# Kernel tuning notes

Hardware: AMD Instinct MI355X
Metric: run time of the kernel (lower is better)

## Reference

```python
import jax, jax.numpy as jnp
import numpy as np

D_MODEL = 512
D_FF = 512
N_EXPERTS = 16
TOP_K = 3
BATCH, SEQ = 1, 2048


def setup_inputs() -> dict:
    key = jax.random.key(0)
    ks = jax.random.split(key, 6)
    x = jax.random.normal(ks[0], (BATCH, SEQ, D_MODEL), dtype=jnp.float32)
    # router gate (std=0.01 per _init_weights)
    gate_w = 0.01 * jax.random.normal(ks[1], (N_EXPERTS, D_MODEL), dtype=jnp.float32)
    expert_bias = jnp.zeros((N_EXPERTS,), dtype=jnp.float32)  # registered buffer, zeros
    # shared SwiGLU expert (std=0.02)
    shared_gate_up = 0.02 * jax.random.normal(ks[2], (2 * D_FF, D_MODEL), dtype=jnp.float32)
    shared_down = 0.02 * jax.random.normal(ks[3], (D_MODEL, D_FF), dtype=jnp.float32)
    # batched routed experts (std=0.02)
    expert_gate_up = 0.02 * jax.random.normal(ks[4], (N_EXPERTS, 2 * D_FF, D_MODEL), dtype=jnp.float32)
    expert_down = 0.02 * jax.random.normal(ks[5], (N_EXPERTS, D_MODEL, D_FF), dtype=jnp.float32)
    return {
        "x": x,
        "gate_w": gate_w,
        "expert_bias": expert_bias,
        "shared_gate_up": shared_gate_up,
        "shared_down": shared_down,
        "expert_gate_up": expert_gate_up,
        "expert_down": expert_down,
    }


def _swiglu(combined):
    gate, up = jnp.split(combined, 2, axis=-1)
    return jax.nn.silu(gate) * up


def reference(x, gate_w, expert_bias, shared_gate_up, shared_down, expert_gate_up, expert_down):
    B, S, D = x.shape
    xf = x.reshape(-1, D)  # [T, D]

    # ---- shared expert (always active) ----
    shared_out = _swiglu(xf @ shared_gate_up.T) @ shared_down.T  # [T, D]

    # ---- router: sigmoid affinity + bias-adjusted top-k ----
    logits = xf @ gate_w.T  # [T, E]
    affinity = jax.nn.sigmoid(logits)
    routing_scores = affinity + expert_bias  # expert_bias buffer (zeros)
    _, sel = jax.lax.top_k(routing_scores, TOP_K)  # [T, K]
    sel_aff = jnp.take_along_axis(affinity, sel, axis=1)  # [T, K]
    gating = sel_aff / (sel_aff.sum(axis=-1, keepdims=True) + 1e-9)  # [T, K]

    # ---- routed experts: per-token SwiGLU with the token's expert weights ----
    # Computed densely per expert then gathered; identical math to the
    # per-token weight-gather in BatchedExperts.
    combined = jnp.einsum('td,efd->tef', xf, expert_gate_up)  # [T, E, 2F]
    hidden = _swiglu(combined)  # [T, E, F]
    expert_out = jnp.einsum('tef,edf->ted', hidden, expert_down)  # [T, E, D]
    sel_out = jnp.take_along_axis(expert_out, sel[:, :, None], axis=1)  # [T, K, D]
    routed_out = jnp.einsum('tk,tkd->td', gating, sel_out)  # [T, D]

    out = shared_out + routed_out  # dropout p=0.0 -> identity
    return out.reshape(B, S, D)
```

## Files before the change

kernel.cpp:

```cpp
#include <hip/hip_runtime.h>

#define T_TOK 2048
#define DM    512
#define DFF   512
#define NE    16

typedef __attribute__((ext_vector_type(8))) short bf16x8;
typedef __attribute__((ext_vector_type(4))) float f32x4;
typedef __attribute__((ext_vector_type(8))) unsigned short us8;

__device__ __forceinline__ unsigned short f2bf(float f) {
  unsigned int u = __float_as_uint(f);
  u += 0x7fffu + ((u >> 16) & 1u);
  return (unsigned short)(u >> 16);
}

__device__ __forceinline__ void dma16(const unsigned short* g, unsigned short* l) {
  __builtin_amdgcn_global_load_lds(
      (const __attribute__((address_space(1))) unsigned int*)g,
      (__attribute__((address_space(3))) unsigned int*)l, 16, 0, 0);
}

#define LDSOFF(row, chunk) ((((row) << 7) + ((((chunk) ^ ((row) & 7))) << 4)))

#define MFMA(a,b,c) __builtin_amdgcn_mfma_f32_16x16x32_bf16((a),(b),(c),0,0,0)

__global__ __launch_bounds__(256) void prep_kernel(
    const float* __restrict__ x, const float* __restrict__ gw,
    const float* __restrict__ bias, int* __restrict__ counts,
    int* __restrict__ list, float* __restrict__ wgt,
    const float* __restrict__ sgu, const float* __restrict__ sdn,
    const float* __restrict__ egu, const float* __restrict__ edn,
    unsigned short* __restrict__ xb,   unsigned short* __restrict__ sgub,
    unsigned short* __restrict__ sdnb, unsigned short* __restrict__ egub,
    unsigned short* __restrict__ ednb, float* __restrict__ out)
{
  const int tid = threadIdx.x;
  if (blockIdx.x >= 512) {
    const int cb = blockIdx.x - 512;
    const int ct = cb * 256 + tid;
    const int CT = 7040 * 256;
    const float4 z4 = {0.f, 0.f, 0.f, 0.f};
    for (int i = ct; i < 262144; i += CT) ((float4*)out)[i] = z4;
    int g = ct;
    const float* s; unsigned short* d; int l;
    if      (g <  131072) { s = x;   d = xb;   l = g;           }
    else if (g <  196608) { s = sgu; d = sgub; l = g -  131072; }
    else if (g <  229376) { s = sdn; d = sdnb; l = g -  196608; }
    else if (g < 1277952) { s = egu; d = egub; l = g -  229376; }
    else                  { s = edn; d = ednb; l = g - 1277952; }
    const float* p = s + (size_t)l * 8;
    float4 v0 = *(const float4*)p;
    float4 v1 = *(const float4*)(p + 4);
    us8 o;
    o[0]=f2bf(v0.x); o[1]=f2bf(v0.y); o[2]=f2bf(v0.z); o[3]=f2bf(v0.w);
    o[4]=f2bf(v1.x); o[5]=f2bf(v1.y); o[6]=f2bf(v1.z); o[7]=f2bf(v1.w);
    *(us8*)(d + (size_t)l * 8) = o;
    return;
  }

  __shared__ float lg[4][16];
  __shared__ int bcnt[16], bbase[16];
  __shared__ int sel_s[4][3], pos_s[4][3];
  __shared__ float g_s[4][3];

  const int w = tid >> 6, lane = tid & 63;
  if (tid < 16) bcnt[tid] = 0;
  const int tok = blockIdx.x * 4 + w;
  const int e = lane & 15, part = lane >> 4;

  const float* xr = x + (size_t)tok * DM + part * 128;
  const float* wr = gw + (size_t)e * DM + part * 128;
  float acc = 0.f;
  #pragma unroll 8
  for (int i = 0; i < 128; i += 4) {
    float4 xv = *(const float4*)(xr + i);
    float4 wv = *(const float4*)(wr + i);
    acc += xv.x*wv.x + xv.y*wv.y + xv.z*wv.z + xv.w*wv.w;
  }
  acc += __shfl_xor(acc, 16);
  acc += __shfl_xor(acc, 32);
  if (lane < 16) lg[w][lane] = 1.f / (1.f + __expf(-acc));
  __syncthreads();

  if (tid < 4) {
    float aff[16], sc[16];
    #pragma unroll
    for (int i = 0; i < 16; ++i) { aff[i] = lg[tid][i]; sc[i] = aff[i] + bias[i]; }
    int sel[3]; float sa[3]; float sum = 0.f;
    #pragma unroll
    for (int k = 0; k < 3; ++k) {
      float best = -1e30f; int bi = 0;
      for (int i = 0; i < 16; ++i) {
        bool used = false;
        for (int j = 0; j < k; ++j) used |= (sel[j] == i);
        if (!used && sc[i] > best) { best = sc[i]; bi = i; }
      }
      sel[k] = bi; sa[k] = aff[bi]; sum += aff[bi];
    }
    float inv = 1.f / (sum + 1e-9f);
    #pragma unroll
    for (int k = 0; k < 3; ++k) {
      int p = atomicAdd(&bcnt[sel[k]], 1);
      sel_s[tid][k] = sel[k]; pos_s[tid][k] = p; g_s[tid][k] = sa[k] * inv;
    }
  }
  __syncthreads();
  if (tid < 16) bbase[tid] = atomicAdd(&counts[tid], bcnt[tid]);
  __syncthreads();
  if (tid < 4) {
    #pragma unroll
    for (int k = 0; k < 3; ++k) {
      int E = sel_s[tid][k];
      int p = bbase[E] + pos_s[tid][k];
      list[E * T_TOK + p] = blockIdx.x * 4 + tid;
      wgt [E * T_TOK + p] = g_s[tid][k];
    }
  }
}

__global__ __launch_bounds__(256, 2) void gemm1_fused(
    const unsigned short* __restrict__ X, const unsigned short* __restrict__ Wsh,
    const unsigned short* __restrict__ Wex, unsigned short* __restrict__ Hall,
    const int* __restrict__ counts, const int* __restrict__ list)
{
  __shared__ unsigned short SA[2][128][64];
  __shared__ unsigned short SG[2][64][64];
  __shared__ unsigned short SU[2][64][64];

  const int n0 = blockIdx.x * 64;
  const int mt = blockIdx.y, z = blockIdx.z;
  int cnt, hb; const unsigned short* W;
  if (z == 0) { cnt = T_TOK; hb = 0; W = Wsh; }
  else {
    const int e = z - 1;
    cnt = counts[e];
    if (mt * 128 >= cnt) return;
    hb = T_TOK;
    for (int i = 0; i < e; ++i) hb += counts[i];
    W = Wex + (size_t)e * (2 * DFF * DM);
  }

  const int tid = threadIdx.x, w = tid >> 6, lane = tid & 63;
  const int rsub = lane >> 3;
  const int cch  = (lane & 7) ^ rsub;
  const unsigned short* ga[4];
  #pragma unroll
  for (int q = 0; q < 4; ++q) {
    int ra = mt * 128 + q * 32 + w * 8 + rsub;
    int rc = ra < cnt ? ra : cnt - 1;
    int tokr = (z == 0) ? rc : list[(z - 1) * T_TOK + rc];
    ga[q] = X + (size_t)tokr * DM + cch * 8;
  }
  const unsigned short *gg[2], *gu[2];
  #pragma unroll
  for (int q = 0; q < 2; ++q) {
    int rb = n0 + q * 32 + w * 8 + rsub;
    gg[q] = W + (size_t)rb * DM + cch * 8;
    gu[q] = W + (size_t)(DFF + rb) * DM + cch * 8;
  }
  unsigned short* lA[2][4]; unsigned short* lG[2][2]; unsigned short* lU[2][2];
  #pragma unroll
  for (int b = 0; b < 2; ++b) {
    #pragma unroll
    for (int q = 0; q < 4; ++q) lA[b][q] = &SA[b][q * 32 + w * 8][0];
    #pragma unroll
    for (int q = 0; q < 2; ++q) {
      lG[b][q] = &SG[b][q * 32 + w * 8][0];
      lU[b][q] = &SU[b][q * 32 + w * 8][0];
    }
  }

  const int wm = (w & 1) * 64;
  const int wn = (w >> 1) * 32;
  const int lr = lane & 15, qd = lane >> 4;
  const char* const sa = (const char*)SA;
  const char* const sg = (const char*)SG;
  const char* const su = (const char*)SU;

  const f32x4 z4 = {0.f, 0.f, 0.f, 0.f};
  f32x4 accg[4][2], accu[4][2];
  #pragma unroll
  for (int i = 0; i < 4; ++i)
    #pragma unroll
    for (int j = 0; j < 2; ++j) { accg[i][j] = z4; accu[i][j] = z4; }

  #pragma unroll
  for (int q = 0; q < 4; ++q) dma16(ga[q], lA[0][q]);
  #pragma unroll
  for (int q = 0; q < 2; ++q) { dma16(gg[q], lG[0][q]); dma16(gu[q], lU[0][q]); }

  #pragma unroll
  for (int i = 0; i < DM / 64; ++i) {
    const int b = i & 1;
    __syncthreads();
    if (i + 1 < DM / 64) {
      const int k1 = (i + 1) * 64, nb = b ^ 1;
      #pragma unroll
      for (int q = 0; q < 4; ++q) dma16(ga[q] + k1, lA[nb][q]);
      #pragma unroll
      for (int q = 0; q < 2; ++q) {
        dma16(gg[q] + k1, lG[nb][q]);
        dma16(gu[q] + k1, lU[nb][q]);
      }
    }
    const int boA = b * 16384;
    const int boB = b * 8192;
    #pragma unroll
    for (int ks = 0; ks < 2; ++ks) {
      const int ch = ks * 4 + qd;
      bf16x8 a[4], g[2], u[2];
      #pragma unroll
      for (int sm = 0; sm < 4; ++sm)
        a[sm] = *(const bf16x8*)(sa + boA + LDSOFF(wm + sm * 16 + lr, ch));
      #pragma unroll
      for (int sn = 0; sn < 2; ++sn) {
        g[sn] = *(const bf16x8*)(sg + boB + LDSOFF(wn + sn * 16 + lr, ch));
        u[sn] = *(const bf16x8*)(su + boB + LDSOFF(wn + sn * 16 + lr, ch));
      }
      #pragma unroll
      for (int sm = 0; sm < 4; ++sm)
        #pragma unroll
        for (int sn = 0; sn < 2; ++sn) {
          accg[sm][sn] = MFMA(a[sm], g[sn], accg[sm][sn]);
          accu[sm][sn] = MFMA(a[sm], u[sn], accu[sm][sn]);
        }
    }
  }

  #pragma unroll
  for (int sm = 0; sm < 4; ++sm)
    #pragma unroll
    for (int sn = 0; sn < 2; ++sn) {
      const int col = n0 + wn + sn * 16 + lr;
      #pragma unroll
      for (int r = 0; r < 4; ++r) {
        const int ent = mt * 128 + wm + sm * 16 + qd * 4 + r;
        if (ent < cnt) {
          float g = accg[sm][sn][r];
          float u = accu[sm][sn][r];
          float h = (g / (1.f + __expf(-g))) * u;
          Hall[(size_t)(hb + ent) * DFF + col] = f2bf(h);
        }
      }
    }
}

__global__ __launch_bounds__(256, 3) void gemm2_fused(
    const unsigned short* __restrict__ Hall, const unsigned short* __restrict__ Wsh,
    const unsigned short* __restrict__ Wex, float* __restrict__ out,
    const int* __restrict__ counts, const int* __restrict__ list,
    const float* __restrict__ wgt)
{
  __shared__ unsigned short SA[2][128][64];
  __shared__ unsigned short SB[2][64][64];

  const int n0 = blockIdx.x * 64;
  const int mt = blockIdx.y, z = blockIdx.z;
  int cnt, hb; const unsigned short* W;
  if (z == 0) { cnt = T_TOK; hb = 0; W = Wsh; }
  else {
    const int e = z - 1;
    cnt = counts[e];
    if (mt * 128 >= cnt) return;
    hb = T_TOK;
    for (int i = 0; i < e; ++i) hb += counts[i];
    W = Wex + (size_t)e * (DM * DFF);
  }

  const int tid = threadIdx.x, w = tid >> 6, lane = tid & 63;
  const int rsub = lane >> 3;
  const int cch  = (lane & 7) ^ rsub;
  const unsigned short* ga[4];
  #pragma unroll
  for (int q = 0; q < 4; ++q) {
    int ra = mt * 128 + q * 32 + w * 8 + rsub;
    int rc = ra < cnt ? ra : cnt - 1;
    ga[q] = Hall + (size_t)(hb + rc) * DFF + cch * 8;
  }
  const unsigned short* gb[2];
  #pragma unroll
  for (int q = 0; q < 2; ++q)
    gb[q] = W + (size_t)(n0 + q * 32 + w * 8 + rsub) * DFF + cch * 8;
  unsigned short* lA[2][4]; unsigned short* lB[2][2];
  #pragma unroll
  for (int b = 0; b < 2; ++b) {
    #pragma unroll
    for (int q = 0; q < 4; ++q) lA[b][q] = &SA[b][q * 32 + w * 8][0];
    #pragma unroll
    for (int q = 0; q < 2; ++q) lB[b][q] = &SB[b][q * 32 + w * 8][0];
  }

  const int wm = (w & 1) * 64;
  const int wn = (w >> 1) * 32;
  const int lr = lane & 15, qd = lane >> 4;
  const char* const sa = (const char*)SA;
  const char* const sb = (const char*)SB;

  const f32x4 z4 = {0.f, 0.f, 0.f, 0.f};
  f32x4 acc[4][2];
  #pragma unroll
  for (int i = 0; i < 4; ++i)
    #pragma unroll
    for (int j = 0; j < 2; ++j) acc[i][j] = z4;

  #pragma unroll
  for (int q = 0; q < 4; ++q) dma16(ga[q], lA[0][q]);
  #pragma unroll
  for (int q = 0; q < 2; ++q) dma16(gb[q], lB[0][q]);

  #pragma unroll
  for (int i = 0; i < DFF / 64; ++i) {
    const int b = i & 1;
    __syncthreads();
    if (i + 1 < DFF / 64) {
      const int k1 = (i + 1) * 64, nb = b ^ 1;
      #pragma unroll
      for (int q = 0; q < 4; ++q) dma16(ga[q] + k1, lA[nb][q]);
      #pragma unroll
      for (int q = 0; q < 2; ++q) dma16(gb[q] + k1, lB[nb][q]);
    }
    const int boA = b * 16384;
    const int boB = b * 8192;
    #pragma unroll
    for (int ks = 0; ks < 2; ++ks) {
      const int ch = ks * 4 + qd;
      bf16x8 a[4], bb[2];
      #pragma unroll
      for (int sm = 0; sm < 4; ++sm)
        a[sm] = *(const bf16x8*)(sa + boA + LDSOFF(wm + sm * 16 + lr, ch));
      #pragma unroll
      for (int sn = 0; sn < 2; ++sn)
        bb[sn] = *(const bf16x8*)(sb + boB + LDSOFF(wn + sn * 16 + lr, ch));
      #pragma unroll
      for (int sm = 0; sm < 4; ++sm)
        #pragma unroll
        for (int sn = 0; sn < 2; ++sn)
          acc[sm][sn] = MFMA(a[sm], bb[sn], acc[sm][sn]);
    }
  }

  #pragma unroll
  for (int sm = 0; sm < 4; ++sm)
    #pragma unroll
    for (int sn = 0; sn < 2; ++sn) {
      const int col = n0 + wn + sn * 16 + lr;
      #pragma unroll
      for (int r = 0; r < 4; ++r) {
        const int ent = mt * 128 + wm + sm * 16 + qd * 4 + r;
        if (ent < cnt) {
          float v = acc[sm][sn][r];
          if (z == 0) {
            atomicAdd(out + (size_t)ent * DM + col, v);
          } else {
            const int   tok = list[(z - 1) * T_TOK + ent];
            const float g   = wgt [(z - 1) * T_TOK + ent];
            atomicAdd(out + (size_t)tok * DM + col, g * v);
          }
        }
      }
    }
}

extern "C" void kernel_launch(void* const* d_in, const int* in_sizes, int n_in,
                              void* d_out, int out_size, void* d_ws, size_t ws_size,
                              hipStream_t stream) {
  const float* x    = (const float*)d_in[0];
  const float* gw   = (const float*)d_in[1];
  const float* bias = (const float*)d_in[2];
  const float* sgu  = (const float*)d_in[3];
  const float* sdn  = (const float*)d_in[4];
  const float* egu  = (const float*)d_in[5];
  const float* edn  = (const float*)d_in[6];
  float* out = (float*)d_out;

  char* ws = (char*)d_ws;
  int*            counts = (int*)(ws + 0);
  int*            list   = (int*)(ws + 64);
  float*          wgt    = (float*)(ws + 131136);
  unsigned short* Hall   = (unsigned short*)(ws + 262208);
  unsigned short* xb     = (unsigned short*)(ws + 8650816);
  unsigned short* sgub   = (unsigned short*)(ws + 10747968);
  unsigned short* sdnb   = (unsigned short*)(ws + 11796544);
  unsigned short* egub   = (unsigned short*)(ws + 12320832);
  unsigned short* ednb   = (unsigned short*)(ws + 29098048);
  const size_t need = 37486656;
  if (ws_size < need) return;

  hipMemsetAsync(counts, 0, 64, stream);
  prep_kernel<<<512 + 7040, 256, 0, stream>>>(
      x, gw, bias, counts, list, wgt, sgu, sdn, egu, edn,
      xb, sgub, sdnb, egub, ednb, out);
  gemm1_fused<<<dim3(8, 16, NE + 1), 256, 0, stream>>>(xb, sgub, egub, Hall, counts, list);
  gemm2_fused<<<dim3(8, 16, NE + 1), 256, 0, stream>>>(Hall, sdnb, ednb, out, counts, list, wgt);
}
```

Measured before the change: 168.4 us.

## Fuse fp32-to-bf16 conversion into GEMM tile loads, drop pre-conversion pass

Removes the separate pass in the prep kernel that converted x and all expert/shared weights to bf16 in workspace. The GEMM kernels now load fp32 tiles into registers, pack them to bf16 and store them into swizzled LDS themselves, replacing the async global-to-LDS DMA for those operands. This saves a full read and write of about 36MB of converted data. In exchange the GEMMs read twice the bytes per tile, repeat the conversion for every tile that reuses a weight or activation row, and lose the asynchronous LDS DMA path, with more register pressure.

```diff
diff --git a/kernel.cpp b/kernel.cpp
--- a/kernel.cpp
+++ b/kernel.cpp
@@ -15,6 +15,13 @@
   return (unsigned short)(u >> 16);
 }
 
+__device__ __forceinline__ us8 pack8(float4 v0, float4 v1) {
+  us8 o;
+  o[0]=f2bf(v0.x); o[1]=f2bf(v0.y); o[2]=f2bf(v0.z); o[3]=f2bf(v0.w);
+  o[4]=f2bf(v1.x); o[5]=f2bf(v1.y); o[6]=f2bf(v1.z); o[7]=f2bf(v1.w);
+  return o;
+}
+
 __device__ __forceinline__ void dma16(const unsigned short* g, unsigned short* l) {
   __builtin_amdgcn_global_load_lds(
       (const __attribute__((address_space(1))) unsigned int*)g,
@@ -29,34 +36,14 @@
     const float* __restrict__ x, const float* __restrict__ gw,
     const float* __restrict__ bias, int* __restrict__ counts,
     int* __restrict__ list, float* __restrict__ wgt,
-    const float* __restrict__ sgu, const float* __restrict__ sdn,
-    const float* __restrict__ egu, const float* __restrict__ edn,
-    unsigned short* __restrict__ xb,   unsigned short* __restrict__ sgub,
-    unsigned short* __restrict__ sdnb, unsigned short* __restrict__ egub,
-    unsigned short* __restrict__ ednb, float* __restrict__ out)
+    float* __restrict__ out)
 {
   const int tid = threadIdx.x;
-  if (blockIdx.x >= 512) {
-    const int cb = blockIdx.x - 512;
-    const int ct = cb * 256 + tid;
-    const int CT = 7040 * 256;
+  {
+    const int g = blockIdx.x * 256 + tid;
     const float4 z4 = {0.f, 0.f, 0.f, 0.f};
-    for (int i = ct; i < 262144; i += CT) ((float4*)out)[i] = z4;
-    int g = ct;
-    const float* s; unsigned short* d; int l;
-    if      (g <  131072) { s = x;   d = xb;   l = g;           }
-    else if (g <  196608) { s = sgu; d = sgub; l = g -  131072; }
-    else if (g <  229376) { s = sdn; d = sdnb; l = g -  196608; }
-    else if (g < 1277952) { s = egu; d = egub; l = g -  229376; }
-    else                  { s = edn; d = ednb; l = g - 1277952; }
-    const float* p = s + (size_t)l * 8;
-    float4 v0 = *(const float4*)p;
-    float4 v1 = *(const float4*)(p + 4);
-    us8 o;
-    o[0]=f2bf(v0.x); o[1]=f2bf(v0.y); o[2]=f2bf(v0.z); o[3]=f2bf(v0.w);
-    o[4]=f2bf(v1.x); o[5]=f2bf(v1.y); o[6]=f2bf(v1.z); o[7]=f2bf(v1.w);
-    *(us8*)(d + (size_t)l * 8) = o;
-    return;
+    ((float4*)out)[g] = z4;
+    ((float4*)out)[g + 131072] = z4;
   }
 
   __shared__ float lg[4][16];
@@ -120,8 +107,8 @@
 }
 
 __global__ __launch_bounds__(256, 2) void gemm1_fused(
-    const unsigned short* __restrict__ X, const unsigned short* __restrict__ Wsh,
-    const unsigned short* __restrict__ Wex, unsigned short* __restrict__ Hall,
+    const float* __restrict__ X, const float* __restrict__ Wsh,
+    const float* __restrict__ Wex, unsigned short* __restrict__ Hall,
     const int* __restrict__ counts, const int* __restrict__ list)
 {
   __shared__ unsigned short SA[2][128][64];
@@ -130,7 +117,7 @@
 
   const int n0 = blockIdx.x * 64;
   const int mt = blockIdx.y, z = blockIdx.z;
-  int cnt, hb; const unsigned short* W;
+  int cnt, hb; const float* W;
   if (z == 0) { cnt = T_TOK; hb = 0; W = Wsh; }
   else {
     const int e = z - 1;
@@ -143,31 +130,33 @@
 
   const int tid = threadIdx.x, w = tid >> 6, lane = tid & 63;
   const int rsub = lane >> 3;
-  const int cch  = (lane & 7) ^ rsub;
-  const unsigned short* ga[4];
+  const int c    = lane & 7;
+
+  const float* gA[4];
+  unsigned short* lA[2][4];
   #pragma unroll
   for (int q = 0; q < 4; ++q) {
-    int ra = mt * 128 + q * 32 + w * 8 + rsub;
+    const int rA = q * 32 + w * 8 + rsub;
+    int ra = mt * 128 + rA;
     int rc = ra < cnt ? ra : cnt - 1;
     int tokr = (z == 0) ? rc : list[(z - 1) * T_TOK + rc];
-    ga[q] = X + (size_t)tokr * DM + cch * 8;
-  }
-  const unsigned short *gg[2], *gu[2];
+    gA[q] = X + (size_t)tokr * DM + c * 8;
+    #pragma unroll
+    for (int b = 0; b < 2; ++b)
+      lA[b][q] = &SA[b][rA][0] + ((c ^ (rA & 7)) << 3);
+  }
+  const float *gG[2], *gU[2];
+  unsigned short *lG[2][2], *lU[2][2];
   #pragma unroll
   for (int q = 0; q < 2; ++q) {
-    int rb = n0 + q * 32 + w * 8 + rsub;
-    gg[q] = W + (size_t)rb * DM + cch * 8;
-    gu[q] = W + (size_t)(DFF + rb) * DM + cch * 8;
-  }
-  unsigned short* lA[2][4]; unsigned short* lG[2][2]; unsigned short* lU[2][2];
-  #pragma unroll
-  for (int b = 0; b < 2; ++b) {
-    #pragma unroll
-    for (int q = 0; q < 4; ++q) lA[b][q] = &SA[b][q * 32 + w * 8][0];
-    #pragma unroll
-    for (int q = 0; q < 2; ++q) {
-      lG[b][q] = &SG[b][q * 32 + w * 8][0];
-      lU[b][q] = &SU[b][q * 32 + w * 8][0];
+    const int rB = q * 32 + w * 8 + rsub;
+    const int rb = n0 + rB;
+    gG[q] = W + (size_t)rb * DM + c * 8;
+    gU[q] = W + (size_t)(DFF + rb) * DM + c * 8;
+    #pragma unroll
+    for (int b = 0; b < 2; ++b) {
+      lG[b][q] = &SG[b][rB][0] + ((c ^ (rB & 7)) << 3);
+      lU[b][q] = &SU[b][rB][0] + ((c ^ (rB & 7)) << 3);
     }
   }
 
@@ -185,23 +174,42 @@
     #pragma unroll
     for (int j = 0; j < 2; ++j) { accg[i][j] = z4; accu[i][j] = z4; }
 
-  #pragma unroll
-  for (int q = 0; q < 4; ++q) dma16(ga[q], lA[0][q]);
-  #pragma unroll
-  for (int q = 0; q < 2; ++q) { dma16(gg[q], lG[0][q]); dma16(gu[q], lU[0][q]); }
+  float4 av0[4], av1[4], gv0[2], gv1[2], uv0[2], uv1[2];
+
+  #pragma unroll
+  for (int q = 0; q < 4; ++q) {
+    av0[q] = *(const float4*)gA[q]; av1[q] = *(const float4*)(gA[q] + 4);
+  }
+  #pragma unroll
+  for (int q = 0; q < 2; ++q) {
+    gv0[q] = *(const float4*)gG[q]; gv1[q] = *(const float4*)(gG[q] + 4);
+    uv0[q] = *(const float4*)gU[q]; uv1[q] = *(const float4*)(gU[q] + 4);
+  }
+  #pragma unroll
+  for (int q = 0; q < 4; ++q) *(us8*)lA[0][q] = pack8(av0[q], av1[q]);
+  #pragma unroll
+  for (int q = 0; q < 2; ++q) {
+    *(us8*)lG[0][q] = pack8(gv0[q], gv1[q]);
+    *(us8*)lU[0][q] = pack8(uv0[q], uv1[q]);
+  }
 
   #pragma unroll
   for (int i = 0; i < DM / 64; ++i) {
     const int b = i & 1;
     __syncthreads();
     if (i + 1 < DM / 64) {
-      const int k1 = (i + 1) * 64, nb = b ^ 1;
-      #pragma unroll
-      for (int q = 0; q < 4; ++q) dma16(ga[q] + k1, lA[nb][q]);
+      const int k1 = (i + 1) * 64;
+      #pragma unroll
+      for (int q = 0; q < 4; ++q) {
+        av0[q] = *(const float4*)(gA[q] + k1);
+        av1[q] = *(const float4*)(gA[q] + k1 + 4);
+      }
       #pragma unroll
       for (int q = 0; q < 2; ++q) {
-        dma16(gg[q] + k1, lG[nb][q]);
-        dma16(gu[q] + k1, lU[nb][q]);
+        gv0[q] = *(const float4*)(gG[q] + k1);
+        gv1[q] = *(const float4*)(gG[q] + k1 + 4);
+        uv0[q] = *(const float4*)(gU[q] + k1);
+        uv1[q] = *(const float4*)(gU[q] + k1 + 4);
       }
     }
     const int boA = b * 16384;
@@ -225,6 +233,16 @@
           accg[sm][sn] = MFMA(a[sm], g[sn], accg[sm][sn]);
           accu[sm][sn] = MFMA(a[sm], u[sn], accu[sm][sn]);
         }
+    }
+    if (i + 1 < DM / 64) {
+      const int nb = b ^ 1;
+      #pragma unroll
+      for (int q = 0; q < 4; ++q) *(us8*)lA[nb][q] = pack8(av0[q], av1[q]);
+      #pragma unroll
+      for (int q = 0; q < 2; ++q) {
+        *(us8*)lG[nb][q] = pack8(gv0[q], gv1[q]);
+        *(us8*)lU[nb][q] = pack8(uv0[q], uv1[q]);
+      }
     }
   }
 
@@ -247,8 +265,8 @@
 }
 
 __global__ __launch_bounds__(256, 3) void gemm2_fused(
-    const unsigned short* __restrict__ Hall, const unsigned short* __restrict__ Wsh,
-    const unsigned short* __restrict__ Wex, float* __restrict__ out,
+    const unsigned short* __restrict__ Hall, const float* __restrict__ Wsh,
+    const float* __restrict__ Wex, float* __restrict__ out,
     const int* __restrict__ counts, const int* __restrict__ list,
     const float* __restrict__ wgt)
 {
@@ -257,7 +275,7 @@
 
   const int n0 = blockIdx.x * 64;
   const int mt = blockIdx.y, z = blockIdx.z;
-  int cnt, hb; const unsigned short* W;
+  int cnt, hb; const float* W;
   if (z == 0) { cnt = T_TOK; hb = 0; W = Wsh; }
   else {
     const int e = z - 1;
@@ -270,25 +288,29 @@
 
   const int tid = threadIdx.x, w = tid >> 6, lane = tid & 63;
   const int rsub = lane >> 3;
-  const int cch  = (lane & 7) ^ rsub;
+  const int c    = lane & 7;
+  const int cch  = c ^ rsub;
+
   const unsigned short* ga[4];
+  unsigned short* lA[2][4];
   #pragma unroll
   for (int q = 0; q < 4; ++q) {
     int ra = mt * 128 + q * 32 + w * 8 + rsub;
     int rc = ra < cnt ? ra : cnt - 1;
     ga[q] = Hall + (size_t)(hb + rc) * DFF + cch * 8;
-  }
-  const unsigned short* gb[2];
-  #pragma unroll
-  for (int q = 0; q < 2; ++q)
-    gb[q] = W + (size_t)(n0 + q * 32 + w * 8 + rsub) * DFF + cch * 8;
-  unsigned short* lA[2][4]; unsigned short* lB[2][2];
-  #pragma unroll
-  for (int b = 0; b < 2; ++b) {
-    #pragma unroll
-    for (int q = 0; q < 4; ++q) lA[b][q] = &SA[b][q * 32 + w * 8][0];
-    #pragma unroll
-    for (int q = 0; q < 2; ++q) lB[b][q] = &SB[b][q * 32 + w * 8][0];
+    #pragma unroll
+    for (int b = 0; b < 2; ++b)
+      lA[b][q] = &SA[b][q * 32 + w * 8][0];
+  }
+  const float* gB[2];
+  unsigned short* lB[2][2];
+  #pragma unroll
+  for (int q = 0; q < 2; ++q) {
+    const int rB = q * 32 + w * 8 + rsub;
+    gB[q] = W + (size_t)(n0 + rB) * DFF + c * 8;
+    #pragma unroll
+    for (int b = 0; b < 2; ++b)
+      lB[b][q] = &SB[b][rB][0] + ((c ^ (rB & 7)) << 3);
   }
 
   const int wm = (w & 1) * 64;
@@ -304,10 +326,16 @@
     #pragma unroll
     for (int j = 0; j < 2; ++j) acc[i][j] = z4;
 
+  float4 bv0[2], bv1[2];
+
   #pragma unroll
   for (int q = 0; q < 4; ++q) dma16(ga[q], lA[0][q]);
   #pragma unroll
-  for (int q = 0; q < 2; ++q) dma16(gb[q], lB[0][q]);
+  for (int q = 0; q < 2; ++q) {
+    bv0[q] = *(const float4*)gB[q]; bv1[q] = *(const float4*)(gB[q] + 4);
+  }
+  #pragma unroll
+  for (int q = 0; q < 2; ++q) *(us8*)lB[0][q] = pack8(bv0[q], bv1[q]);
 
   #pragma unroll
   for (int i = 0; i < DFF / 64; ++i) {
@@ -318,7 +346,10 @@
       #pragma unroll
       for (int q = 0; q < 4; ++q) dma16(ga[q] + k1, lA[nb][q]);
       #pragma unroll
-      for (int q = 0; q < 2; ++q) dma16(gb[q] + k1, lB[nb][q]);
+      for (int q = 0; q < 2; ++q) {
+        bv0[q] = *(const float4*)(gB[q] + k1);
+        bv1[q] = *(const float4*)(gB[q] + k1 + 4);
+      }
     }
     const int boA = b * 16384;
     const int boB = b * 8192;
@@ -337,6 +368,11 @@
         #pragma unroll
         for (int sn = 0; sn < 2; ++sn)
           acc[sm][sn] = MFMA(a[sm], bb[sn], acc[sm][sn]);
+    }
+    if (i + 1 < DFF / 64) {
+      const int nb = b ^ 1;
+      #pragma unroll
+      for (int q = 0; q < 2; ++q) *(us8*)lB[nb][q] = pack8(bv0[q], bv1[q]);
     }
   }
 
@@ -379,18 +415,11 @@
   int*            list   = (int*)(ws + 64);
   float*          wgt    = (float*)(ws + 131136);
   unsigned short* Hall   = (unsigned short*)(ws + 262208);
-  unsigned short* xb     = (unsigned short*)(ws + 8650816);
-  unsigned short* sgub   = (unsigned short*)(ws + 10747968);
-  unsigned short* sdnb   = (unsigned short*)(ws + 11796544);
-  unsigned short* egub   = (unsigned short*)(ws + 12320832);
-  unsigned short* ednb   = (unsigned short*)(ws + 29098048);
-  const size_t need = 37486656;
+  const size_t need = 8650816;
   if (ws_size < need) return;
 
   hipMemsetAsync(counts, 0, 64, stream);
-  prep_kernel<<<512 + 7040, 256, 0, stream>>>(
-      x, gw, bias, counts, list, wgt, sgu, sdn, egu, edn,
-      xb, sgub, sdnb, egub, ednb, out);
-  gemm1_fused<<<dim3(8, 16, NE + 1), 256, 0, stream>>>(xb, sgub, egub, Hall, counts, list);
-  gemm2_fused<<<dim3(8, 16, NE + 1), 256, 0, stream>>>(Hall, sdnb, ednb, out, counts, list, wgt);
-}
+  prep_kernel<<<512, 256, 0, stream>>>(x, gw, bias, counts, list, wgt, out);
+  gemm1_fused<<<dim3(8, 16, NE + 1), 256, 0, stream>>>(x, sgu, egu, Hall, counts, list);
+  gemm2_fused<<<dim3(8, 16, NE + 1), 256, 0, stream>>>(Hall, sdn, edn, out, counts, list, wgt);
+}
```

Measured after the change: 178.4 us. +6.0%, slower.

## Split MoE GEMM tiles across 8 waves and overlap down-weight conversion with gemm1

Applied to the files above, without the earlier changes.

Both GEMM kernels move to 512-thread blocks. In gemm1, half the waves compute the gate tile and half the up tile, and the up results pass through LDS to the gate waves for the SwiGLU epilogue. In gemm2, each wave's N tile is halved. The conversion of the down-projection weights to bf16 and the zeroing of the output move out of the prep kernel into an extra z-slice of gemm1, which shortens the prep grid and lets that work overlap with the first GEMM. The aim is more waves in flight and fewer accumulator registers per wave, at the cost of an extra LDS round trip and barrier, and the converted down weights must finish before gemm2 reads them.

```diff
diff --git a/kernel.cpp b/kernel.cpp
--- a/kernel.cpp
+++ b/kernel.cpp
@@ -15,6 +15,13 @@
   return (unsigned short)(u >> 16);
 }
 
+__device__ __forceinline__ us8 pack8(float4 v0, float4 v1) {
+  us8 o;
+  o[0]=f2bf(v0.x); o[1]=f2bf(v0.y); o[2]=f2bf(v0.z); o[3]=f2bf(v0.w);
+  o[4]=f2bf(v1.x); o[5]=f2bf(v1.y); o[6]=f2bf(v1.z); o[7]=f2bf(v1.w);
+  return o;
+}
+
 __device__ __forceinline__ void dma16(const unsigned short* g, unsigned short* l) {
   __builtin_amdgcn_global_load_lds(
       (const __attribute__((address_space(1))) unsigned int*)g,
@@ -29,33 +36,21 @@
     const float* __restrict__ x, const float* __restrict__ gw,
     const float* __restrict__ bias, int* __restrict__ counts,
     int* __restrict__ list, float* __restrict__ wgt,
-    const float* __restrict__ sgu, const float* __restrict__ sdn,
-    const float* __restrict__ egu, const float* __restrict__ edn,
-    unsigned short* __restrict__ xb,   unsigned short* __restrict__ sgub,
-    unsigned short* __restrict__ sdnb, unsigned short* __restrict__ egub,
-    unsigned short* __restrict__ ednb, float* __restrict__ out)
+    const float* __restrict__ sgu, const float* __restrict__ egu,
+    unsigned short* __restrict__ xb, unsigned short* __restrict__ sgub,
+    unsigned short* __restrict__ egub)
 {
   const int tid = threadIdx.x;
   if (blockIdx.x >= 512) {
-    const int cb = blockIdx.x - 512;
-    const int ct = cb * 256 + tid;
-    const int CT = 7040 * 256;
-    const float4 z4 = {0.f, 0.f, 0.f, 0.f};
-    for (int i = ct; i < 262144; i += CT) ((float4*)out)[i] = z4;
-    int g = ct;
+    const int g = (blockIdx.x - 512) * 256 + tid;
     const float* s; unsigned short* d; int l;
-    if      (g <  131072) { s = x;   d = xb;   l = g;           }
-    else if (g <  196608) { s = sgu; d = sgub; l = g -  131072; }
-    else if (g <  229376) { s = sdn; d = sdnb; l = g -  196608; }
-    else if (g < 1277952) { s = egu; d = egub; l = g -  229376; }
-    else                  { s = edn; d = ednb; l = g - 1277952; }
+    if      (g <  131072) { s = x;   d = xb;   l = g;          }
+    else if (g <  196608) { s = sgu; d = sgub; l = g - 131072; }
+    else                  { s = egu; d = egub; l = g - 196608; }
     const float* p = s + (size_t)l * 8;
     float4 v0 = *(const float4*)p;
     float4 v1 = *(const float4*)(p + 4);
-    us8 o;
-    o[0]=f2bf(v0.x); o[1]=f2bf(v0.y); o[2]=f2bf(v0.z); o[3]=f2bf(v0.w);
-    o[4]=f2bf(v1.x); o[5]=f2bf(v1.y); o[6]=f2bf(v1.z); o[7]=f2bf(v1.w);
-    *(us8*)(d + (size_t)l * 8) = o;
+    *(us8*)(d + (size_t)l * 8) = pack8(v0, v1);
     return;
   }
 
@@ -119,17 +114,38 @@
   }
 }
 
-__global__ __launch_bounds__(256, 2) void gemm1_fused(
+__global__ __launch_bounds__(512, 4) void gemm1_fused(
     const unsigned short* __restrict__ X, const unsigned short* __restrict__ Wsh,
     const unsigned short* __restrict__ Wex, unsigned short* __restrict__ Hall,
-    const int* __restrict__ counts, const int* __restrict__ list)
+    const int* __restrict__ counts, const int* __restrict__ list,
+    const float* __restrict__ sdn, const float* __restrict__ edn,
+    unsigned short* __restrict__ sdnb, unsigned short* __restrict__ ednb,
+    float* __restrict__ out)
 {
-  __shared__ unsigned short SA[2][128][64];
-  __shared__ unsigned short SG[2][64][64];
-  __shared__ unsigned short SU[2][64][64];
+  const int tid = threadIdx.x;
+  const int z = blockIdx.z;
+
+  if (z == NE + 1) {
+    const int t = (blockIdx.y * 8 + blockIdx.x) * 512 + tid;
+    const float4 z4 = {0.f, 0.f, 0.f, 0.f};
+    #pragma unroll
+    for (int i = 0; i < 4; ++i) ((float4*)out)[t + i * 65536] = z4;
+    for (int g = t; g < 557056; g += 65536) {
+      const float* s; unsigned short* d; int l;
+      if (g < 32768) { s = sdn; d = sdnb; l = g; }
+      else           { s = edn; d = ednb; l = g - 32768; }
+      const float* p = s + (size_t)l * 8;
+      float4 v0 = *(const float4*)p;
+      float4 v1 = *(const float4*)(p + 4);
+      *(us8*)(d + (size_t)l * 8) = pack8(v0, v1);
+    }
+    return;
+  }
+
+  __shared__ __align__(1024) char smem[65536];
 
   const int n0 = blockIdx.x * 64;
-  const int mt = blockIdx.y, z = blockIdx.z;
+  const int mt = blockIdx.y;
   int cnt, hb; const unsigned short* W;
   if (z == 0) { cnt = T_TOK; hb = 0; W = Wsh; }
   else {
@@ -141,119 +157,123 @@
     W = Wex + (size_t)e * (2 * DFF * DM);
   }
 
-  const int tid = threadIdx.x, w = tid >> 6, lane = tid & 63;
-  const int rsub = lane >> 3;
-  const int cch  = (lane & 7) ^ rsub;
-  const unsigned short* ga[4];
-  #pragma unroll
-  for (int q = 0; q < 4; ++q) {
-    int ra = mt * 128 + q * 32 + w * 8 + rsub;
+  const int w = tid >> 6, lane = tid & 63;
+  const bool is_u = w >= 4;
+  const int wv = w & 3;
+
+  const int rA0 = w * 16 + (lane >> 3);
+  const int cchA = (lane & 7) ^ (lane >> 3);
+  const unsigned short* ga[2];
+  #pragma unroll
+  for (int q = 0; q < 2; ++q) {
+    int ra = mt * 128 + rA0 + q * 8;
     int rc = ra < cnt ? ra : cnt - 1;
     int tokr = (z == 0) ? rc : list[(z - 1) * T_TOK + rc];
-    ga[q] = X + (size_t)tokr * DM + cch * 8;
-  }
-  const unsigned short *gg[2], *gu[2];
+    ga[q] = X + (size_t)tokr * DM + cchA * 8;
+  }
+  const int rB0 = wv * 16 + (lane >> 3);
+  const unsigned short* gb[2];
   #pragma unroll
   for (int q = 0; q < 2; ++q) {
-    int rb = n0 + q * 32 + w * 8 + rsub;
-    gg[q] = W + (size_t)rb * DM + cch * 8;
-    gu[q] = W + (size_t)(DFF + rb) * DM + cch * 8;
-  }
-  unsigned short* lA[2][4]; unsigned short* lG[2][2]; unsigned short* lU[2][2];
-  #pragma unroll
-  for (int b = 0; b < 2; ++b) {
-    #pragma unroll
-    for (int q = 0; q < 4; ++q) lA[b][q] = &SA[b][q * 32 + w * 8][0];
+    int rb = n0 + rB0 + q * 8;
+    gb[q] = W + (size_t)(is_u ? DFF + rb : rb) * DM + cchA * 8;
+  }
+  const int bb0 = is_u ? 49152 : 32768;
+  unsigned short* lA[2][2]; unsigned short* lB[2][2];
+  #pragma unroll
+  for (int b = 0; b < 2; ++b)
     #pragma unroll
     for (int q = 0; q < 2; ++q) {
-      lG[b][q] = &SG[b][q * 32 + w * 8][0];
-      lU[b][q] = &SU[b][q * 32 + w * 8][0];
-    }
-  }
-
-  const int wm = (w & 1) * 64;
-  const int wn = (w >> 1) * 32;
+      lA[b][q] = (unsigned short*)(smem + b * 16384) + (w * 16 + q * 8) * 64;
+      lB[b][q] = (unsigned short*)(smem + bb0 + b * 8192) + (wv * 16 + q * 8) * 64;
+    }
+
+  const int wm = (wv & 1) * 64;
+  const int wn = (wv >> 1) * 32;
   const int lr = lane & 15, qd = lane >> 4;
-  const char* const sa = (const char*)SA;
-  const char* const sg = (const char*)SG;
-  const char* const su = (const char*)SU;
 
   const f32x4 z4 = {0.f, 0.f, 0.f, 0.f};
-  f32x4 accg[4][2], accu[4][2];
+  f32x4 acc[4][2];
   #pragma unroll
   for (int i = 0; i < 4; ++i)
     #pragma unroll
-    for (int j = 0; j < 2; ++j) { accg[i][j] = z4; accu[i][j] = z4; }
-
-  #pragma unroll
-  for (int q = 0; q < 4; ++q) dma16(ga[q], lA[0][q]);
-  #pragma unroll
-  for (int q = 0; q < 2; ++q) { dma16(gg[q], lG[0][q]); dma16(gu[q], lU[0][q]); }
+    for (int j = 0; j < 2; ++j) acc[i][j] = z4;
+
+  #pragma unroll
+  for (int q = 0; q < 2; ++q) { dma16(ga[q], lA[0][q]); dma16(gb[q], lB[0][q]); }
 
   #pragma unroll
   for (int i = 0; i < DM / 64; ++i) {
-    const int b = i & 1;
     __syncthreads();
     if (i + 1 < DM / 64) {
-      const int k1 = (i + 1) * 64, nb = b ^ 1;
-      #pragma unroll
-      for (int q = 0; q < 4; ++q) dma16(ga[q] + k1, lA[nb][q]);
+      const int k1 = (i + 1) * 64, nb = (i + 1) & 1;
       #pragma unroll
       for (int q = 0; q < 2; ++q) {
-        dma16(gg[q] + k1, lG[nb][q]);
-        dma16(gu[q] + k1, lU[nb][q]);
+        dma16(ga[q] + k1, lA[nb][q]);
+        dma16(gb[q] + k1, lB[nb][q]);
       }
     }
-    const int boA = b * 16384;
-    const int boB = b * 8192;
+    const int boA = (i & 1) * 16384;
+    const int boB = bb0 + (i & 1) * 8192;
     #pragma unroll
     for (int ks = 0; ks < 2; ++ks) {
       const int ch = ks * 4 + qd;
-      bf16x8 a[4], g[2], u[2];
+      bf16x8 a[4], bv[2];
       #pragma unroll
       for (int sm = 0; sm < 4; ++sm)
-        a[sm] = *(const bf16x8*)(sa + boA + LDSOFF(wm + sm * 16 + lr, ch));
-      #pragma unroll
-      for (int sn = 0; sn < 2; ++sn) {
-        g[sn] = *(const bf16x8*)(sg + boB + LDSOFF(wn + sn * 16 + lr, ch));
-        u[sn] = *(const bf16x8*)(su + boB + LDSOFF(wn + sn * 16 + lr, ch));
-      }
+        a[sm] = *(const bf16x8*)(smem + boA + LDSOFF(wm + sm * 16 + lr, ch));
+      #pragma unroll
+      for (int sn = 0; sn < 2; ++sn)
+        bv[sn] = *(const bf16x8*)(smem + boB + LDSOFF(wn + sn * 16 + lr, ch));
       #pragma unroll
       for (int sm = 0; sm < 4; ++sm)
         #pragma unroll
-        for (int sn = 0; sn < 2; ++sn) {
-          accg[sm][sn] = MFMA(a[sm], g[sn], accg[sm][sn]);
-          accu[sm][sn] = MFMA(a[sm], u[sn], accu[sm][sn]);
-        }
-    }
-  }
-
-  #pragma unroll
-  for (int sm = 0; sm < 4; ++sm)
-    #pragma unroll
-    for (int sn = 0; sn < 2; ++sn) {
-      const int col = n0 + wn + sn * 16 + lr;
-      #pragma unroll
-      for (int r = 0; r < 4; ++r) {
-        const int ent = mt * 128 + wm + sm * 16 + qd * 4 + r;
-        if (ent < cnt) {
-          float g = accg[sm][sn][r];
-          float u = accu[sm][sn][r];
-          float h = (g / (1.f + __expf(-g))) * u;
-          Hall[(size_t)(hb + ent) * DFF + col] = f2bf(h);
+        for (int sn = 0; sn < 2; ++sn)
+          acc[sm][sn] = MFMA(a[sm], bv[sn], acc[sm][sn]);
+    }
+  }
+
+  __syncthreads();
+  float* const us = (float*)smem;
+  if (is_u) {
+    #pragma unroll
+    for (int sm = 0; sm < 4; ++sm)
+      #pragma unroll
+      for (int sn = 0; sn < 2; ++sn) {
+        const int col = wn + sn * 16 + lr;
+        #pragma unroll
+        for (int r = 0; r < 4; ++r)
+          us[(wm + sm * 16 + qd * 4 + r) * 65 + col] = acc[sm][sn][r];
+      }
+  }
+  __syncthreads();
+  if (!is_u) {
+    #pragma unroll
+    for (int sm = 0; sm < 4; ++sm)
+      #pragma unroll
+      for (int sn = 0; sn < 2; ++sn) {
+        const int col = n0 + wn + sn * 16 + lr;
+        #pragma unroll
+        for (int r = 0; r < 4; ++r) {
+          const int ent = mt * 128 + wm + sm * 16 + qd * 4 + r;
+          if (ent < cnt) {
+            float g = acc[sm][sn][r];
+            float u = us[(wm + sm * 16 + qd * 4 + r) * 65 + wn + sn * 16 + lr];
+            float h = (g / (1.f + __expf(-g))) * u;
+            Hall[(size_t)(hb + ent) * DFF + col] = f2bf(h);
+          }
         }
       }
-    }
-}
-
-__global__ __launch_bounds__(256, 3) void gemm2_fused(
+  }
+}
+
+__global__ __launch_bounds__(512, 4) void gemm2_fused(
     const unsigned short* __restrict__ Hall, const unsigned short* __restrict__ Wsh,
     const unsigned short* __restrict__ Wex, float* __restrict__ out,
     const int* __restrict__ counts, const int* __restrict__ list,
     const float* __restrict__ wgt)
 {
-  __shared__ unsigned short SA[2][128][64];
-  __shared__ unsigned short SB[2][64][64];
+  __shared__ __align__(1024) char smem[49152];
 
   const int n0 = blockIdx.x * 64;
   const int mt = blockIdx.y, z = blockIdx.z;
@@ -269,97 +289,83 @@
   }
 
   const int tid = threadIdx.x, w = tid >> 6, lane = tid & 63;
-  const int rsub = lane >> 3;
-  const int cch  = (lane & 7) ^ rsub;
-  const unsigned short* ga[4];
-  #pragma unroll
-  for (int q = 0; q < 4; ++q) {
-    int ra = mt * 128 + q * 32 + w * 8 + rsub;
+  const int rA0 = w * 16 + (lane >> 3);
+  const int cchA = (lane & 7) ^ (lane >> 3);
+  const unsigned short* ga[2];
+  #pragma unroll
+  for (int q = 0; q < 2; ++q) {
+    int ra = mt * 128 + rA0 + q * 8;
     int rc = ra < cnt ? ra : cnt - 1;
-    ga[q] = Hall + (size_t)(hb + rc) * DFF + cch * 8;
-  }
-  const unsigned short* gb[2];
-  #pragma unroll
-  for (int q = 0; q < 2; ++q)
-    gb[q] = W + (size_t)(n0 + q * 32 + w * 8 + rsub) * DFF + cch * 8;
-  unsigned short* lA[2][4]; unsigned short* lB[2][2];
+    ga[q] = Hall + (size_t)(hb + rc) * DFF + cchA * 8;
+  }
+  const int rB0 = w * 8 + (lane >> 3);
+  const unsigned short* gb = W + (size_t)(n0 + rB0) * DFF + cchA * 8;
+
+  unsigned short* lA[2][2]; unsigned short* lB[2];
   #pragma unroll
   for (int b = 0; b < 2; ++b) {
     #pragma unroll
-    for (int q = 0; q < 4; ++q) lA[b][q] = &SA[b][q * 32 + w * 8][0];
-    #pragma unroll
-    for (int q = 0; q < 2; ++q) lB[b][q] = &SB[b][q * 32 + w * 8][0];
+    for (int q = 0; q < 2; ++q)
+      lA[b][q] = (unsigned short*)(smem + b * 16384) + (w * 16 + q * 8) * 64;
+    lB[b] = (unsigned short*)(smem + 32768 + b * 8192) + (w * 8) * 64;
   }
 
   const int wm = (w & 1) * 64;
-  const int wn = (w >> 1) * 32;
+  const int wn = (w >> 1) * 16;
   const int lr = lane & 15, qd = lane >> 4;
-  const char* const sa = (const char*)SA;
-  const char* const sb = (const char*)SB;
 
   const f32x4 z4 = {0.f, 0.f, 0.f, 0.f};
-  f32x4 acc[4][2];
-  #pragma unroll
-  for (int i = 0; i < 4; ++i)
-    #pragma unroll
-    for (int j = 0; j < 2; ++j) acc[i][j] = z4;
-
-  #pragma unroll
-  for (int q = 0; q < 4; ++q) dma16(ga[q], lA[0][q]);
-  #pragma unroll
-  for (int q = 0; q < 2; ++q) dma16(gb[q], lB[0][q]);
+  f32x4 acc[4];
+  #pragma unroll
+  for (int i = 0; i < 4; ++i) acc[i] = z4;
+
+  #pragma unroll
+  for (int q = 0; q < 2; ++q) dma16(ga[q], lA[0][q]);
+  dma16(gb, lB[0]);
 
   #pragma unroll
   for (int i = 0; i < DFF / 64; ++i) {
-    const int b = i & 1;
     __syncthreads();
     if (i + 1 < DFF / 64) {
-      const int k1 = (i + 1) * 64, nb = b ^ 1;
-      #pragma unroll
-      for (int q = 0; q < 4; ++q) dma16(ga[q] + k1, lA[nb][q]);
-      #pragma unroll
-      for (int q = 0; q < 2; ++q) dma16(gb[q] + k1, lB[nb][q]);
-    }
-    const int boA = b * 16384;
-    const int boB = b * 8192;
+      const int k1 = (i + 1) * 64, nb = (i + 1) & 1;
+      #pragma unroll
+      for (int q = 0; q < 2; ++q) dma16(ga[q] + k1, lA[nb][q]);
+      dma16(gb + k1, lB[nb]);
+    }
+    const int boA = (i & 1) * 16384;
+    const int boB = 32768 + (i & 1) * 8192;
     #pragma unroll
     for (int ks = 0; ks < 2; ++ks) {
       const int ch = ks * 4 + qd;
-      bf16x8 a[4], bb[2];
+      bf16x8 a[4];
       #pragma unroll
       for (int sm = 0; sm < 4; ++sm)
-        a[sm] = *(const bf16x8*)(sa + boA + LDSOFF(wm + sm * 16 + lr, ch));
-      #pragma unroll
-      for (int sn = 0; sn < 2; ++sn)
-        bb[sn] = *(const bf16x8*)(sb + boB + LDSOFF(wn + sn * 16 + lr, ch));
+        a[sm] = *(const bf16x8*)(smem + boA + LDSOFF(wm + sm * 16 + lr, ch));
+      bf16x8 bv = *(const bf16x8*)(smem + boB + LDSOFF(wn + lr, ch));
       #pragma unroll
       for (int sm = 0; sm < 4; ++sm)
-        #pragma unroll
-        for (int sn = 0; sn < 2; ++sn)
-          acc[sm][sn] = MFMA(a[sm], bb[sn], acc[sm][sn]);
-    }
-  }
-
-  #pragma unroll
-  for (int sm = 0; sm < 4; ++sm)
-    #pragma unroll
-    for (int sn = 0; sn < 2; ++sn) {
-      const int col = n0 + wn + sn * 16 + lr;
-      #pragma unroll
-      for (int r = 0; r < 4; ++r) {
-        const int ent = mt * 128 + wm + sm * 16 + qd * 4 + r;
-        if (ent < cnt) {
-          float v = acc[sm][sn][r];
-          if (z == 0) {
-            atomicAdd(out + (size_t)ent * DM + col, v);
-          } else {
-            const int   tok = list[(z - 1) * T_TOK + ent];
-            const float g   = wgt [(z - 1) * T_TOK + ent];
-            atomicAdd(out + (size_t)tok * DM + col, g * v);
-          }
+        acc[sm] = MFMA(a[sm], bv, acc[sm]);
+    }
+  }
+
+  #pragma unroll
+  for (int sm = 0; sm < 4; ++sm) {
+    const int col = n0 + wn + lr;
+    #pragma unroll
+    for (int r = 0; r < 4; ++r) {
+      const int ent = mt * 128 + wm + sm * 16 + qd * 4 + r;
+      if (ent < cnt) {
+        float v = acc[sm][r];
+        if (z == 0) {
+          atomicAdd(out + (size_t)ent * DM + col, v);
+        } else {
+          const int   tok = list[(z - 1) * T_TOK + ent];
+          const float g   = wgt [(z - 1) * T_TOK + ent];
+          atomicAdd(out + (size_t)tok * DM + col, g * v);
         }
       }
     }
+  }
 }
 
 extern "C" void kernel_launch(void* const* d_in, const int* in_sizes, int n_in,
@@ -388,9 +394,10 @@
   if (ws_size < need) return;
 
   hipMemsetAsync(counts, 0, 64, stream);
-  prep_kernel<<<512 + 7040, 256, 0, stream>>>(
-      x, gw, bias, counts, list, wgt, sgu, sdn, egu, edn,
-      xb, sgub, sdnb, egub, ednb, out);
-  gemm1_fused<<<dim3(8, 16, NE + 1), 256, 0, stream>>>(xb, sgub, egub, Hall, counts, list);
-  gemm2_fused<<<dim3(8, 16, NE + 1), 256, 0, stream>>>(Hall, sdnb, ednb, out, counts, list, wgt);
-}
+  prep_kernel<<<512 + 4864, 256, 0, stream>>>(
+      x, gw, bias, counts, list, wgt, sgu, egu, xb, sgub, egub);
+  gemm1_fused<<<dim3(8, 16, NE + 2), 512, 0, stream>>>(
+      xb, sgub, egub, Hall, counts, list, sdn, edn, sdnb, ednb, out);
+  gemm2_fused<<<dim3(8, 16, NE + 1), 512, 0, stream>>>(
+      Hall, sdnb, ednb, out, counts, list, wgt);
+}
```

After: 163.7 us. 1.03x faster.
